# Kernel optimization log

Measured on AMD Instinct MI355X. Metric: run time of the kernel, lower is better.

Reference implementation:

```python
import jax, jax.numpy as jnp
import numpy as np

B, S, D, L = 4, 512, 768, 64


def setup_inputs() -> dict:
    key = jax.random.key(0)
    k1, k2, k3, k4, k5 = jax.random.split(key, 5)
    return {
        "head": jax.random.normal(k1, (B, S, D), dtype=jnp.float32),
        "dep": jax.random.normal(k2, (B, S, D), dtype=jnp.float32),
        "label_U_diag": jax.random.normal(k3, (L, D), dtype=jnp.float32) * 0.02,
        "label_W": jax.random.normal(k4, (L, 2 * D), dtype=jnp.float32) * 0.02,
        "label_b": jax.random.normal(k5, (L,), dtype=jnp.float32) * 0.02,
    }


def reference(head, dep, label_U_diag, label_W, label_b):
    # t1[b,l,i,o] = sum_d head[b,i,d] * U[l,d] * dep[b,o,d]  (diag bilinear)
    t1 = jnp.einsum('bid,ld,bod->blio', head, label_U_diag, dep)
    # Linear term: instead of materializing the O(S^2 * 2D) concat tensor,
    # split W into head/dep halves and broadcast-add two O(S*L) matmuls.
    d = head.shape[-1]
    Wh, Wd = label_W[:, :d], label_W[:, d:]
    t2_h = jnp.einsum('bid,ld->bli', head, Wh)  # [B, L, S] (row / head index)
    t2_d = jnp.einsum('bod,ld->blo', dep, Wd)   # [B, L, S] (col / dep index)
    return t1 + t2_h[:, :, :, None] + t2_d[:, :, None, :] + label_b[None, :, None, None]
```

## Files before the change

### kernel.cpp

```cpp
#include <hip/hip_runtime.h>

typedef __bf16 bf16;
typedef __bf16 bf16x8 __attribute__((ext_vector_type(8)));
typedef float  f32x4  __attribute__((ext_vector_type(4)));

#define S 512
#define DD 768
#define LL 64
#define BB 4

__device__ __forceinline__ void async_copy16(const void* g, void* l) {
    __builtin_amdgcn_global_load_lds(
        (const __attribute__((address_space(1))) unsigned int*)g,
        (__attribute__((address_space(3))) unsigned int*)l,
        16, 0, 0);
}

__device__ __forceinline__ bf16x8 scale_cvt(float4 a, float4 b, float4 ua, float4 ub) {
    bf16x8 p;
    p[0] = (bf16)(a.x * ua.x); p[1] = (bf16)(a.y * ua.y);
    p[2] = (bf16)(a.z * ua.z); p[3] = (bf16)(a.w * ua.w);
    p[4] = (bf16)(b.x * ub.x); p[5] = (bf16)(b.y * ub.y);
    p[6] = (bf16)(b.z * ub.z); p[7] = (bf16)(b.w * ub.w);
    return p;
}

__global__ void cvt_dep_kernel(const float* __restrict__ dep, bf16* __restrict__ out) {
    int idx = (blockIdx.x * 256 + threadIdx.x) * 8;
    float4 a = *(const float4*)(dep + idx);
    float4 c = *(const float4*)(dep + idx + 4);
    bf16x8 p;
    p[0] = (bf16)a.x; p[1] = (bf16)a.y; p[2] = (bf16)a.z; p[3] = (bf16)a.w;
    p[4] = (bf16)c.x; p[5] = (bf16)c.y; p[6] = (bf16)c.z; p[7] = (bf16)c.w;
    *(bf16x8*)(out + idx) = p;
}

__global__ void t2_kernel(const float* __restrict__ head, const float* __restrict__ dep,
                          const float* __restrict__ W, const float* __restrict__ bias,
                          float* __restrict__ t2h, float* __restrict__ t2d) {
    __shared__ float Wl[16][DD];
    __shared__ float red[64][4][16];
    int bid = blockIdx.x;
    int sel = bid >> 7;
    int r   = bid & 127;
    int b   = r >> 5;
    int lg  = (r >> 3) & 3;
    int ic  = r & 7;
    const float* src = sel ? dep : head;
    int t = threadIdx.x;

    for (int l16 = 0; l16 < 16; ++l16) {
        const float* wp = W + (size_t)(lg * 16 + l16) * (2 * DD) + sel * DD;
        Wl[l16][t]       = wp[t];
        Wl[l16][t + 256] = wp[t + 256];
        Wl[l16][t + 512] = wp[t + 512];
    }
    __syncthreads();

    int iq = t >> 2, dq = t & 3;
    int i  = ic * 64 + iq;
    const float* rowp = src + (size_t)(b * S + i) * DD;
    float acc[16];
#pragma unroll
    for (int l16 = 0; l16 < 16; ++l16) acc[l16] = 0.f;
    for (int it = 0; it < 48; ++it) {
        int d = dq * 4 + it * 16;
        float4 x = *(const float4*)(rowp + d);
#pragma unroll
        for (int l16 = 0; l16 < 16; ++l16) {
            float4 wv = *(const float4*)&Wl[l16][d];
            acc[l16] += x.x * wv.x + x.y * wv.y + x.z * wv.z + x.w * wv.w;
        }
    }
#pragma unroll
    for (int l16 = 0; l16 < 16; ++l16) red[iq][dq][l16] = acc[l16];
    __syncthreads();

    int iq2 = t >> 2, l4 = t & 3;
    float* dst = sel ? t2d : t2h;
#pragma unroll
    for (int j = 0; j < 4; ++j) {
        int l16 = l4 * 4 + j;
        float v = red[iq2][0][l16] + red[iq2][1][l16] + red[iq2][2][l16] + red[iq2][3][l16];
        if (sel) v += bias[lg * 16 + l16];
        dst[(size_t)(b * LL + lg * 16 + l16) * S + ic * 64 + iq2] = v;
    }
}

__global__ __launch_bounds__(256, 3) void biaffine_main(
    const float* __restrict__ head, const bf16* __restrict__ depb,
    const float* __restrict__ U, const float* __restrict__ t2h,
    const float* __restrict__ t2d, float* __restrict__ out) {
    __shared__ __align__(16) bf16 As[2][128][32];
    __shared__ __align__(16) bf16 Bs[2][128][32];
    __shared__ __align__(16) float Ulds[DD];

    const int tid  = threadIdx.x;
    const int lane = tid & 63;
    const int w    = tid >> 6;
    const int bi0  = (blockIdx.x & 3) << 7;
    const int bo0  = (blockIdx.x >> 2) << 7;
    const int l    = blockIdx.y;
    const int b    = blockIdx.z;

    bf16* AsB = &As[0][0][0];
    bf16* BsB = &Bs[0][0][0];

    {
        const float* up = U + (size_t)l * DD;
        Ulds[tid]       = up[tid];
        Ulds[tid + 256] = up[tid + 256];
        Ulds[tid + 512] = up[tid + 512];
    }

    const int r1 = tid >> 2;
    const int cp = tid & 3;
    const int sw = (r1 >> 1) & 3;
    const int ca = cp ^ sw;
    const float* hp0 = head + (size_t)(b * S + bi0 + r1) * DD + ca * 8;
    const float* hp1 = hp0 + (size_t)64 * DD;
    const int aoff0 = r1 * 32 + cp * 8;
    const int aoff1 = (r1 + 64) * 32 + cp * 8;

    const int rB0 = w * 32 + (lane >> 2);
    const int rB1 = rB0 + 16;
    const int cpB = lane & 3;
    const bf16* bg0 = depb + (size_t)(b * S + bo0 + rB0) * DD + (cpB ^ ((rB0 >> 1) & 3)) * 8;
    const bf16* bg1 = depb + (size_t)(b * S + bo0 + rB1) * DD + (cpB ^ ((rB1 >> 1) & 3)) * 8;
    const int boff0 = (w * 32) * 32;
    const int boff1 = (w * 32 + 16) * 32;

    const int wr = w & 1, wc = w >> 1;
    const int mrow = lane & 15, q = lane >> 4;
    int aFo[4], bFo[4];
#pragma unroll
    for (int mi = 0; mi < 4; ++mi) {
        int rowA = wr * 64 + mi * 16 + mrow;
        aFo[mi] = rowA * 32 + ((q ^ ((rowA >> 1) & 3)) * 8);
        int rowB = wc * 64 + mi * 16 + mrow;
        bFo[mi] = rowB * 32 + ((q ^ ((rowB >> 1) & 3)) * 8);
    }

    f32x4 acc[4][4];
#pragma unroll
    for (int mi = 0; mi < 4; ++mi)
#pragma unroll
        for (int ni = 0; ni < 4; ++ni)
            acc[mi][ni] = (f32x4){0.f, 0.f, 0.f, 0.f};

    float4 h0a = *(const float4*)(hp0);
    float4 h0b = *(const float4*)(hp0 + 4);
    float4 h1a = *(const float4*)(hp1);
    float4 h1b = *(const float4*)(hp1 + 4);
    async_copy16(bg0, BsB + boff0);
    async_copy16(bg1, BsB + boff1);
    __syncthreads();
    {
        const float* uu = &Ulds[ca * 8];
        float4 ua = *(const float4*)(uu);
        float4 ub = *(const float4*)(uu + 4);
        *(bf16x8*)(AsB + aoff0) = scale_cvt(h0a, h0b, ua, ub);
        *(bf16x8*)(AsB + aoff1) = scale_cvt(h1a, h1b, ua, ub);
    }
    __syncthreads();

    for (int kt = 0; kt < 24; ++kt) {
        const int coff = (kt & 1) * 4096;
        const int soff = coff ^ 4096;
        const bool st = kt < 23;

        if (st) {
            const float* h0 = hp0 + (kt + 1) * 32;
            const float* h1 = hp1 + (kt + 1) * 32;
            h0a = *(const float4*)(h0);
            h0b = *(const float4*)(h0 + 4);
            h1a = *(const float4*)(h1);
            h1b = *(const float4*)(h1 + 4);
            async_copy16(bg0 + (kt + 1) * 32, BsB + soff + boff0);
            async_copy16(bg1 + (kt + 1) * 32, BsB + soff + boff1);
        }

        bf16x8 af[4], bfr[4];
#pragma unroll
        for (int mi = 0; mi < 4; ++mi) af[mi]  = *(const bf16x8*)(AsB + coff + aFo[mi]);
#pragma unroll
        for (int ni = 0; ni < 4; ++ni) bfr[ni] = *(const bf16x8*)(BsB + coff + bFo[ni]);
#pragma unroll
        for (int mi = 0; mi < 4; ++mi)
#pragma unroll
            for (int ni = 0; ni < 4; ++ni)
                acc[mi][ni] = __builtin_amdgcn_mfma_f32_16x16x32_bf16(af[mi], bfr[ni], acc[mi][ni], 0, 0, 0);

        if (st) {
            const float* uu = &Ulds[(kt + 1) * 32 + ca * 8];
            float4 ua = *(const float4*)(uu);
            float4 ub = *(const float4*)(uu + 4);
            *(bf16x8*)(AsB + soff + aoff0) = scale_cvt(h0a, h0b, ua, ub);
            *(bf16x8*)(AsB + soff + aoff1) = scale_cvt(h1a, h1b, ua, ub);
        }
        __syncthreads();
    }

    const size_t bl = (size_t)(b * LL + l);
    const float* t2hp = t2h + bl * S + bi0 + wr * 64;
    const float* t2dp = t2d + bl * S + bo0 + wc * 64;
    float* outbase = out + bl * (size_t)(S * S);
#pragma unroll
    for (int mi = 0; mi < 4; ++mi) {
        float4 th = *(const float4*)&t2hp[mi * 16 + q * 4];
        int row0 = bi0 + wr * 64 + mi * 16 + q * 4;
#pragma unroll
        for (int ni = 0; ni < 4; ++ni) {
            int col = bo0 + wc * 64 + ni * 16 + mrow;
            float td = t2dp[ni * 16 + mrow];
            float* op = outbase + (size_t)row0 * S + col;
            op[0 * S] = acc[mi][ni][0] + th.x + td;
            op[1 * S] = acc[mi][ni][1] + th.y + td;
            op[2 * S] = acc[mi][ni][2] + th.z + td;
            op[3 * S] = acc[mi][ni][3] + th.w + td;
        }
    }
}

extern "C" void kernel_launch(void* const* d_in, const int* in_sizes, int n_in,
                              void* d_out, int out_size, void* d_ws, size_t ws_size,
                              hipStream_t stream) {
    const float* head = (const float*)d_in[0];
    const float* dep  = (const float*)d_in[1];
    const float* U    = (const float*)d_in[2];
    const float* W    = (const float*)d_in[3];
    const float* bias = (const float*)d_in[4];
    float* out = (float*)d_out;

    char*  ws   = (char*)d_ws;
    bf16*  depb = (bf16*)ws;
    float* t2h  = (float*)(ws + 3145728);
    float* t2d  = (float*)(ws + 3145728 + 524288);

    cvt_dep_kernel<<<768, 256, 0, stream>>>(dep, depb);
    t2_kernel<<<256, 256, 0, stream>>>(head, dep, W, bias, t2h, t2d);
    biaffine_main<<<dim3(16, LL, BB), 256, 0, stream>>>(head, depb, U, t2h, t2d, out);
}
```

Measured before the change: 389.4 us.

## Triple-buffer LDS tiles with prefetch distance two in biaffine main loop

The main GEMM loop moves from double to triple LDS buffering. Loads for tile k+2 are issued while tile k is computed, and tile k+1 is converted and scaled from registers that alternate between two sets. The loop is unrolled by two and uses explicit s_waitcnt vmcnt/lgkmcnt plus s_barrier in place of __syncthreads, so only the older transfers are waited on. The aim is to hide more global-load latency behind the MFMA work, at the cost of more LDS per block and more live registers.

```diff
diff --git a/kernel.cpp b/kernel.cpp
--- a/kernel.cpp
+++ b/kernel.cpp
@@ -87,12 +87,60 @@
     }
 }
 
+__device__ __forceinline__ void substep(
+    int k, int cOff, int nOff, int sOff,
+    const float* hp0, const float* hp1, const bf16* bg0, const bf16* bg1,
+    bf16* AsB, bf16* BsB, const float* Ulds,
+    int boff0, int boff1, int aoff0, int aoff1, int ca,
+    const int* aFo, const int* bFo,
+    float4& L0, float4& L1, float4& L2, float4& L3,
+    float4& W0, float4& W1, float4& W2, float4& W3,
+    f32x4 (&acc)[4][4])
+{
+    const bool stg = (k + 2) < 24;
+    if (stg) {
+        async_copy16(bg0 + (k + 2) * 32, BsB + sOff + boff0);
+        async_copy16(bg1 + (k + 2) * 32, BsB + sOff + boff1);
+        const float* h0 = hp0 + (k + 2) * 32;
+        const float* h1 = hp1 + (k + 2) * 32;
+        L0 = *(const float4*)(h0);
+        L1 = *(const float4*)(h0 + 4);
+        L2 = *(const float4*)(h1);
+        L3 = *(const float4*)(h1 + 4);
+    }
+
+    bf16x8 af[4], bfr[4];
+#pragma unroll
+    for (int mi = 0; mi < 4; ++mi) af[mi]  = *(const bf16x8*)(AsB + cOff + aFo[mi]);
+#pragma unroll
+    for (int ni = 0; ni < 4; ++ni) bfr[ni] = *(const bf16x8*)(BsB + cOff + bFo[ni]);
+#pragma unroll
+    for (int mi = 0; mi < 4; ++mi)
+#pragma unroll
+        for (int ni = 0; ni < 4; ++ni)
+            acc[mi][ni] = __builtin_amdgcn_mfma_f32_16x16x32_bf16(af[mi], bfr[ni], acc[mi][ni], 0, 0, 0);
+
+    if (k + 1 < 24) {
+        const float* uu = &Ulds[(k + 1) * 32 + ca * 8];
+        float4 ua = *(const float4*)(uu);
+        float4 ub = *(const float4*)(uu + 4);
+        *(bf16x8*)(AsB + nOff + aoff0) = scale_cvt(W0, W1, ua, ub);
+        *(bf16x8*)(AsB + nOff + aoff1) = scale_cvt(W2, W3, ua, ub);
+    }
+
+    if (k < 23) {
+        if (stg) { asm volatile("s_waitcnt vmcnt(6) lgkmcnt(0)" ::: "memory"); }
+        else     { asm volatile("s_waitcnt vmcnt(0) lgkmcnt(0)" ::: "memory"); }
+        __builtin_amdgcn_s_barrier();
+    }
+}
+
 __global__ __launch_bounds__(256, 3) void biaffine_main(
     const float* __restrict__ head, const bf16* __restrict__ depb,
     const float* __restrict__ U, const float* __restrict__ t2h,
     const float* __restrict__ t2d, float* __restrict__ out) {
-    __shared__ __align__(16) bf16 As[2][128][32];
-    __shared__ __align__(16) bf16 Bs[2][128][32];
+    __shared__ __align__(16) bf16 As[3][128][32];
+    __shared__ __align__(16) bf16 Bs[3][128][32];
     __shared__ __align__(16) float Ulds[DD];
 
     const int tid  = threadIdx.x;
@@ -148,57 +196,44 @@
         for (int ni = 0; ni < 4; ++ni)
             acc[mi][ni] = (f32x4){0.f, 0.f, 0.f, 0.f};
 
-    float4 h0a = *(const float4*)(hp0);
-    float4 h0b = *(const float4*)(hp0 + 4);
-    float4 h1a = *(const float4*)(hp1);
-    float4 h1b = *(const float4*)(hp1 + 4);
-    async_copy16(bg0, BsB + boff0);
-    async_copy16(bg1, BsB + boff1);
+    float4 aP0, aP1, aP2, aP3;
+    float4 aQ0, aQ1, aQ2, aQ3;
+
+    aP0 = *(const float4*)(hp0);      aP1 = *(const float4*)(hp0 + 4);
+    aP2 = *(const float4*)(hp1);      aP3 = *(const float4*)(hp1 + 4);
+    aQ0 = *(const float4*)(hp0 + 32); aQ1 = *(const float4*)(hp0 + 36);
+    aQ2 = *(const float4*)(hp1 + 32); aQ3 = *(const float4*)(hp1 + 36);
+    async_copy16(bg0,      BsB + boff0);
+    async_copy16(bg1,      BsB + boff1);
+    async_copy16(bg0 + 32, BsB + 4096 + boff0);
+    async_copy16(bg1 + 32, BsB + 4096 + boff1);
     __syncthreads();
     {
-        const float* uu = &Ulds[ca * 8];
-        float4 ua = *(const float4*)(uu);
-        float4 ub = *(const float4*)(uu + 4);
-        *(bf16x8*)(AsB + aoff0) = scale_cvt(h0a, h0b, ua, ub);
-        *(bf16x8*)(AsB + aoff1) = scale_cvt(h1a, h1b, ua, ub);
-    }
-    __syncthreads();
-
-    for (int kt = 0; kt < 24; ++kt) {
-        const int coff = (kt & 1) * 4096;
-        const int soff = coff ^ 4096;
-        const bool st = kt < 23;
-
-        if (st) {
-            const float* h0 = hp0 + (kt + 1) * 32;
-            const float* h1 = hp1 + (kt + 1) * 32;
-            h0a = *(const float4*)(h0);
-            h0b = *(const float4*)(h0 + 4);
-            h1a = *(const float4*)(h1);
-            h1b = *(const float4*)(h1 + 4);
-            async_copy16(bg0 + (kt + 1) * 32, BsB + soff + boff0);
-            async_copy16(bg1 + (kt + 1) * 32, BsB + soff + boff1);
-        }
-
-        bf16x8 af[4], bfr[4];
-#pragma unroll
-        for (int mi = 0; mi < 4; ++mi) af[mi]  = *(const bf16x8*)(AsB + coff + aFo[mi]);
-#pragma unroll
-        for (int ni = 0; ni < 4; ++ni) bfr[ni] = *(const bf16x8*)(BsB + coff + bFo[ni]);
-#pragma unroll
-        for (int mi = 0; mi < 4; ++mi)
-#pragma unroll
-            for (int ni = 0; ni < 4; ++ni)
-                acc[mi][ni] = __builtin_amdgcn_mfma_f32_16x16x32_bf16(af[mi], bfr[ni], acc[mi][ni], 0, 0, 0);
-
-        if (st) {
-            const float* uu = &Ulds[(kt + 1) * 32 + ca * 8];
-            float4 ua = *(const float4*)(uu);
-            float4 ub = *(const float4*)(uu + 4);
-            *(bf16x8*)(AsB + soff + aoff0) = scale_cvt(h0a, h0b, ua, ub);
-            *(bf16x8*)(AsB + soff + aoff1) = scale_cvt(h1a, h1b, ua, ub);
-        }
-        __syncthreads();
+        const float* uu0 = &Ulds[ca * 8];
+        float4 ua = *(const float4*)(uu0);
+        float4 ub = *(const float4*)(uu0 + 4);
+        *(bf16x8*)(AsB + aoff0) = scale_cvt(aP0, aP1, ua, ub);
+        *(bf16x8*)(AsB + aoff1) = scale_cvt(aP2, aP3, ua, ub);
+        const float* uu1 = &Ulds[32 + ca * 8];
+        float4 uc = *(const float4*)(uu1);
+        float4 ud = *(const float4*)(uu1 + 4);
+        *(bf16x8*)(AsB + 4096 + aoff0) = scale_cvt(aQ0, aQ1, uc, ud);
+        *(bf16x8*)(AsB + 4096 + aoff1) = scale_cvt(aQ2, aQ3, uc, ud);
+    }
+    asm volatile("s_waitcnt lgkmcnt(0)" ::: "memory");
+    __builtin_amdgcn_s_barrier();
+
+    int cOff = 0, nOff = 4096, sOff = 8192;
+#pragma unroll 1
+    for (int kt = 0; kt < 24; kt += 2) {
+        substep(kt, cOff, nOff, sOff, hp0, hp1, bg0, bg1, AsB, BsB, Ulds,
+                boff0, boff1, aoff0, aoff1, ca, aFo, bFo,
+                aP0, aP1, aP2, aP3, aQ0, aQ1, aQ2, aQ3, acc);
+        { int t0 = cOff; cOff = nOff; nOff = sOff; sOff = t0; }
+        substep(kt + 1, cOff, nOff, sOff, hp0, hp1, bg0, bg1, AsB, BsB, Ulds,
+                boff0, boff1, aoff0, aoff1, ca, aFo, bFo,
+                aQ0, aQ1, aQ2, aQ3, aP0, aP1, aP2, aP3, acc);
+        { int t0 = cOff; cOff = nOff; nOff = sOff; sOff = t0; }
     }
 
     const size_t bl = (size_t)(b * LL + l);
```

After: 413.6 us. +6.2%, slower.

## Load dep MFMA fragments directly from global instead of staging through LDS

Applied to the files above, without the earlier changes.

Removes the B-operand shared-memory buffer and async global-to-LDS copies; each wave now reads its bf16 dep fragments straight from global memory inside the k-loop. This halves LDS usage and raises the launch-bounds occupancy target from 3 to 4 blocks per CU. In exchange, fragments are fetched redundantly by waves sharing columns, and load latency is no longer hidden by a double-buffered prefetch.

```diff
diff --git a/kernel.cpp b/kernel.cpp
--- a/kernel.cpp
+++ b/kernel.cpp
@@ -8,13 +8,6 @@
 #define DD 768
 #define LL 64
 #define BB 4
-
-__device__ __forceinline__ void async_copy16(const void* g, void* l) {
-    __builtin_amdgcn_global_load_lds(
-        (const __attribute__((address_space(1))) unsigned int*)g,
-        (__attribute__((address_space(3))) unsigned int*)l,
-        16, 0, 0);
-}
 
 __device__ __forceinline__ bf16x8 scale_cvt(float4 a, float4 b, float4 ua, float4 ub) {
     bf16x8 p;
@@ -87,12 +80,11 @@
     }
 }
 
-__global__ __launch_bounds__(256, 3) void biaffine_main(
+__global__ __launch_bounds__(256, 4) void biaffine_main(
     const float* __restrict__ head, const bf16* __restrict__ depb,
     const float* __restrict__ U, const float* __restrict__ t2h,
     const float* __restrict__ t2d, float* __restrict__ out) {
     __shared__ __align__(16) bf16 As[2][128][32];
-    __shared__ __align__(16) bf16 Bs[2][128][32];
     __shared__ __align__(16) float Ulds[DD];
 
     const int tid  = threadIdx.x;
@@ -104,7 +96,6 @@
     const int b    = blockIdx.z;
 
     bf16* AsB = &As[0][0][0];
-    bf16* BsB = &Bs[0][0][0];
 
     {
         const float* up = U + (size_t)l * DD;
@@ -122,24 +113,20 @@
     const int aoff0 = r1 * 32 + cp * 8;
     const int aoff1 = (r1 + 64) * 32 + cp * 8;
 
-    const int rB0 = w * 32 + (lane >> 2);
-    const int rB1 = rB0 + 16;
-    const int cpB = lane & 3;
-    const bf16* bg0 = depb + (size_t)(b * S + bo0 + rB0) * DD + (cpB ^ ((rB0 >> 1) & 3)) * 8;
-    const bf16* bg1 = depb + (size_t)(b * S + bo0 + rB1) * DD + (cpB ^ ((rB1 >> 1) & 3)) * 8;
-    const int boff0 = (w * 32) * 32;
-    const int boff1 = (w * 32 + 16) * 32;
-
     const int wr = w & 1, wc = w >> 1;
     const int mrow = lane & 15, q = lane >> 4;
-    int aFo[4], bFo[4];
+
+    int aFo[4];
 #pragma unroll
     for (int mi = 0; mi < 4; ++mi) {
         int rowA = wr * 64 + mi * 16 + mrow;
         aFo[mi] = rowA * 32 + ((q ^ ((rowA >> 1) & 3)) * 8);
-        int rowB = wc * 64 + mi * 16 + mrow;
-        bFo[mi] = rowB * 32 + ((q ^ ((rowB >> 1) & 3)) * 8);
-    }
+    }
+
+    const bf16* bgf0 = depb + (size_t)(b * S + bo0 + wc * 64 +  0 + mrow) * DD + q * 8;
+    const bf16* bgf1 = depb + (size_t)(b * S + bo0 + wc * 64 + 16 + mrow) * DD + q * 8;
+    const bf16* bgf2 = depb + (size_t)(b * S + bo0 + wc * 64 + 32 + mrow) * DD + q * 8;
+    const bf16* bgf3 = depb + (size_t)(b * S + bo0 + wc * 64 + 48 + mrow) * DD + q * 8;
 
     f32x4 acc[4][4];
 #pragma unroll
@@ -152,8 +139,6 @@
     float4 h0b = *(const float4*)(hp0 + 4);
     float4 h1a = *(const float4*)(hp1);
     float4 h1b = *(const float4*)(hp1 + 4);
-    async_copy16(bg0, BsB + boff0);
-    async_copy16(bg1, BsB + boff1);
     __syncthreads();
     {
         const float* uu = &Ulds[ca * 8];
@@ -176,15 +161,18 @@
             h0b = *(const float4*)(h0 + 4);
             h1a = *(const float4*)(h1);
             h1b = *(const float4*)(h1 + 4);
-            async_copy16(bg0 + (kt + 1) * 32, BsB + soff + boff0);
-            async_copy16(bg1 + (kt + 1) * 32, BsB + soff + boff1);
-        }
-
-        bf16x8 af[4], bfr[4];
-#pragma unroll
-        for (int mi = 0; mi < 4; ++mi) af[mi]  = *(const bf16x8*)(AsB + coff + aFo[mi]);
-#pragma unroll
-        for (int ni = 0; ni < 4; ++ni) bfr[ni] = *(const bf16x8*)(BsB + coff + bFo[ni]);
+        }
+
+        bf16x8 bfr[4];
+        bfr[0] = *(const bf16x8*)(bgf0 + kt * 32);
+        bfr[1] = *(const bf16x8*)(bgf1 + kt * 32);
+        bfr[2] = *(const bf16x8*)(bgf2 + kt * 32);
+        bfr[3] = *(const bf16x8*)(bgf3 + kt * 32);
+
+        bf16x8 af[4];
+#pragma unroll
+        for (int mi = 0; mi < 4; ++mi) af[mi] = *(const bf16x8*)(AsB + coff + aFo[mi]);
+
 #pragma unroll
         for (int mi = 0; mi < 4; ++mi)
 #pragma unroll
```

Result: slower. 493.3 us (+26.7%).
